# Performance work log

Measured on AMD Instinct MI355X. Metric: run time of the kernel, lower is better.

Reference implementation:

```python
import jax, jax.numpy as jnp
import numpy as np

B, S, D_IN, D_ST = 4, 4096, 1024, 1024


def setup_inputs() -> dict:
    key = jax.random.key(0)
    ks = jax.random.split(key, 7)
    s_in = 1.0 / np.sqrt(D_IN)
    s_st = 1.0 / np.sqrt(D_ST)
    return {
        "x": jax.random.normal(ks[0], (B, S, D_IN), dtype=jnp.float32),
        "gate_w": jax.random.uniform(ks[1], (D_IN, D_ST), jnp.float32, -s_in, s_in),
        "gate_b": jax.random.uniform(ks[2], (D_ST,), jnp.float32, -s_in, s_in),
        "inp_w": jax.random.uniform(ks[3], (D_IN, D_ST), jnp.float32, -s_in, s_in),
        "inp_b": jax.random.uniform(ks[4], (D_ST,), jnp.float32, -s_in, s_in),
        "out_w": jax.random.uniform(ks[5], (D_ST, D_IN), jnp.float32, -s_st, s_st),
        "out_b": jax.random.uniform(ks[6], (D_IN,), jnp.float32, -s_st, s_st),
    }


def reference(x, gate_w, gate_b, inp_w, inp_b, out_w, out_b):
    # x: [B, S, D_in]
    inp = jnp.einsum("bsd,de->bse", x, inp_w) + inp_b      # [B,S,Dst]
    gate = jax.nn.sigmoid(jnp.einsum("bsd,de->bse", x, gate_w) + gate_b)
    b_t = (1.0 - gate) * inp                               # [B,S,Dst]

    # affine recurrence h_t = gate_t * h_{t-1} + b_t via lax.scan over time
    def step(h, ab):
        a, b = ab
        h = a * h + b
        return h, h

    a_sb = jnp.swapaxes(gate, 0, 1)  # [S,B,Dst]
    b_sb = jnp.swapaxes(b_t, 0, 1)
    h0 = jnp.zeros((x.shape[0], inp.shape[-1]), dtype=x.dtype)
    _, hs = jax.lax.scan(step, h0, (a_sb, b_sb))           # [S,B,Dst]
    scan_out = jnp.swapaxes(hs, 0, 1)                      # [B,S,Dst]

    return x + jnp.einsum("bse,ed->bsd", scan_out, out_w) + out_b
```

## Files before the change

kernel.cpp:

```cpp
#include <hip/hip_runtime.h>

typedef unsigned short u16;
typedef unsigned int   u32;
typedef __bf16 bf16x8 __attribute__((ext_vector_type(8)));
typedef float  f32x4  __attribute__((ext_vector_type(4)));

#define DEVI __device__ __forceinline__

DEVI u16 f2bf(float f) {
    union { float f; u32 u; } c; c.f = f;
    u32 u = c.u;
    u32 r = (u + 0x7fffu + ((u >> 16) & 1u)) >> 16;
    return (u16)r;
}
DEVI float bf2f(u16 v) {
    union { u32 u; float f; } c; c.u = ((u32)v) << 16;
    return c.f;
}

DEVI void gload16(const void* g, void* l) {
    __builtin_amdgcn_global_load_lds(
        (const __attribute__((address_space(1))) void*)g,
        (__attribute__((address_space(3))) void*)l, 16, 0, 0);
}


#define VMW(N)  asm volatile("s_waitcnt vmcnt(" #N ")" ::: "memory")
#define BAR     __builtin_amdgcn_s_barrier()
#define SP1     __builtin_amdgcn_s_setprio(1)
#define SP0     __builtin_amdgcn_s_setprio(0)
#define CLOSE(N) __builtin_amdgcn_sched_barrier(0); VMW(N); BAR
#define CLOSEB   __builtin_amdgcn_sched_barrier(0); BAR

DEVI void stage_kh(const u16* g, u16* slot, int tid) {
    const int K = 1024;
    const int wvb = (tid >> 6) << 9;
    const int r = tid >> 2;
    const int p = tid & 3;
    const int c = p ^ (r & 3);
    const long off = (long)r * K + (c << 3);
    gload16(g + off, slot + wvb);
    gload16(g + off + (long)128 * K, slot + 4096 + wvb);
}

DEVI void ld4(bf16x8 (&d)[4], const u16* p) {
#pragma unroll
    for (int q = 0; q < 4; ++q) d[q] = *(const bf16x8*)(p + q * 512);
}
DEVI void mm16(f32x4 (&acc)[8][4], const bf16x8 a[4], const bf16x8 b[4], int mh) {
#pragma unroll
    for (int q = 0; q < 4; ++q)
#pragma unroll
        for (int n = 0; n < 4; ++n)
            acc[mh * 4 + q][n] =
                __builtin_amdgcn_mfma_f32_16x16x32_bf16(a[q], b[n], acc[mh * 4 + q][n], 0, 0, 0);
}

DEVI void pipeline(const u16* Ablk, const u16* Bblk, u16* lds,
                   f32x4 (&acc)[8][4], int tid) {
    const int lane = tid & 63;
    const int wm = (tid >> 6) >> 2, wn = (tid >> 6) & 3;
    const int pch = ((lane >> 4) ^ (lane & 3)) << 3;
    const int aoff = wm * 4096 + (lane & 15) * 32 + pch;
    const int boff = wn * 2048 + (lane & 15) * 32 + pch;

    stage_kh(Bblk,      lds + 16384, tid);
    stage_kh(Ablk,      lds + 0,     tid);
    stage_kh(Bblk + 32, lds + 24576, tid);
    stage_kh(Ablk + 32, lds + 8192,  tid);
    stage_kh(Bblk + 64, lds + 49152, tid);
    stage_kh(Ablk + 64, lds + 32768, tid);
    stage_kh(Bblk + 96, lds + 57344, tid);
    VMW(10); BAR;

    bf16x8 afA[4], afB[4], bfr[4];
    ld4(afA, lds + aoff);

#pragma unroll 1
    for (int j = 0; j < 7; ++j) {
        const u16* Aod = Ablk + (2 * j + 1) * 64;
        const u16* At2 = Ablk + (2 * j + 2) * 64;
        const u16* Bt2 = Bblk + (2 * j + 2) * 64;
        ld4(bfr, lds + 16384 + boff);
        ld4(afB, lds + 2048 + aoff);
        stage_kh(Aod + 32, lds + 40960, tid);
        SP1; mm16(acc, afA, bfr, 0); SP0; CLOSE(8);
        ld4(afA, lds + 8192 + aoff);
        stage_kh(Bt2, lds + 16384, tid);
        SP1; mm16(acc, afB, bfr, 1); SP0; CLOSE(8);
        ld4(bfr, lds + 24576 + boff);
        ld4(afB, lds + 10240 + aoff);
        stage_kh(At2, lds + 0, tid);
        SP1; mm16(acc, afA, bfr, 0); SP0; CLOSE(8);
        ld4(afA, lds + 32768 + aoff);
        stage_kh(Bt2 + 32, lds + 24576, tid);
        SP1; mm16(acc, afB, bfr, 1); SP0; CLOSE(8);
        ld4(bfr, lds + 49152 + boff);
        ld4(afB, lds + 34816 + aoff);
        stage_kh(At2 + 32, lds + 8192, tid);
        SP1; mm16(acc, afA, bfr, 0); SP0; CLOSE(8);
        ld4(afA, lds + 40960 + aoff);
        stage_kh(Bt2 + 64, lds + 49152, tid);
        SP1; mm16(acc, afB, bfr, 1); SP0; CLOSE(8);
        ld4(bfr, lds + 57344 + boff);
        ld4(afB, lds + 43008 + aoff);
        stage_kh(At2 + 64, lds + 32768, tid);
        SP1; mm16(acc, afA, bfr, 0); SP0; CLOSE(8);
        ld4(afA, lds + aoff);
        stage_kh(Bt2 + 96, lds + 57344, tid);
        SP1; mm16(acc, afB, bfr, 1); SP0; CLOSE(8);
    }
    {
        const u16* Aod = Ablk + 15 * 64;
        ld4(bfr, lds + 16384 + boff);
        ld4(afB, lds + 2048 + aoff);
        stage_kh(Aod + 32, lds + 40960, tid);
        SP1; mm16(acc, afA, bfr, 0); SP0; CLOSE(8);
        ld4(afA, lds + 8192 + aoff);
        SP1; mm16(acc, afB, bfr, 1); SP0; CLOSEB;
        ld4(bfr, lds + 24576 + boff);
        ld4(afB, lds + 10240 + aoff);
        SP1; mm16(acc, afA, bfr, 0); SP0; CLOSE(4);
        ld4(afA, lds + 32768 + aoff);
        SP1; mm16(acc, afB, bfr, 1); SP0; CLOSEB;
        ld4(bfr, lds + 49152 + boff);
        ld4(afB, lds + 34816 + aoff);
        SP1; mm16(acc, afA, bfr, 0); SP0; CLOSE(0);
        ld4(afA, lds + 40960 + aoff);
        SP1; mm16(acc, afB, bfr, 1); SP0; CLOSEB;
        ld4(bfr, lds + 57344 + boff);
        ld4(afB, lds + 43008 + aoff);
        SP1; mm16(acc, afA, bfr, 0); SP0; CLOSEB;
        SP1; mm16(acc, afB, bfr, 1); SP0;
    }
}


__global__ __launch_bounds__(512, 2) void k_gemm_cat8(
    const u16* __restrict__ A, const u16* __restrict__ Bcat,
    const float* __restrict__ gb, const float* __restrict__ ib,
    u32* __restrict__ ab) {
    __shared__ __align__(16) u16 lds[65536];
    const int tid = threadIdx.x, lane = tid & 63;
    const int wm = (tid >> 6) >> 2, wn = (tid >> 6) & 3;

    int fid = (int)blockIdx.y * 8 + (int)blockIdx.x;
    int swz = (fid & 7) * 64 + (fid >> 3);
    const long bn = swz & 7, bm = swz >> 3;

    f32x4 acc[8][4] = {};
    pipeline(A + bm * 256 * 1024, Bcat + bn * 256 * 1024, lds, acc, tid);

    const long rbase = bm * 256 + wm * 128;
    const int chbase = (int)bn * 128 + wn * 32;
#pragma unroll
    for (int t = 0; t < 2; ++t) {
        int ch = chbase + t * 16 + (lane & 15);
        float g0 = gb[ch], i0 = ib[ch];
#pragma unroll
        for (int m = 0; m < 8; ++m) {
            long row = rbase + m * 16 + ((lane >> 4) << 2);
#pragma unroll
            for (int i = 0; i < 4; ++i) {
                float pg = acc[m][2 * t][i] + g0;
                float pi = acc[m][2 * t + 1][i] + i0;
                float aa = 1.0f / (1.0f + __expf(-pg));
                float bb = (1.0f - aa) * pi;
                ab[(row + i) * 1024 + ch] = (u32)f2bf(aa) | ((u32)f2bf(bb) << 16);
            }
        }
    }
}


__global__ __launch_bounds__(512, 2) void k_gemm_out8(
    const u16* __restrict__ A, const u16* __restrict__ Bt,
    const float* __restrict__ xres, const float* __restrict__ ob,
    float* __restrict__ out) {
    __shared__ __align__(16) u16 lds[65536];
    const int tid = threadIdx.x, lane = tid & 63;
    const int wm = (tid >> 6) >> 2, wn = (tid >> 6) & 3;

    int fid = (int)blockIdx.y * 4 + (int)blockIdx.x;
    int swz = (fid & 7) * 32 + (fid >> 3);
    const long bn = swz & 3, bm = swz >> 2;

    f32x4 acc[8][4] = {};
    pipeline(A + bm * 256 * 1024, Bt + bn * 256 * 1024, lds, acc, tid);

    const long rbase = bm * 256 + wm * 128;
    const int cbase = (int)bn * 256 + wn * 64;
#pragma unroll
    for (int n = 0; n < 4; ++n) {
        int col = cbase + n * 16 + (lane & 15);
        float o0 = ob[col];
#pragma unroll
        for (int m = 0; m < 8; ++m) {
            long row = rbase + m * 16 + ((lane >> 4) << 2);
#pragma unroll
            for (int i = 0; i < 4; ++i) {
                long o = (row + i) * 1024 + col;
                out[o] = acc[m][n][i] + o0 + xres[o];
            }
        }
    }
}


__global__ __launch_bounds__(256) void k_cvt_x(const float4* __restrict__ x,
                                               uint2* __restrict__ o, int n4) {
    int i = blockIdx.x * 256 + threadIdx.x;
    if (i < n4) {
        float4 v = x[i];
        uint2 r;
        r.x = (u32)f2bf(v.x) | ((u32)f2bf(v.y) << 16);
        r.y = (u32)f2bf(v.z) | ((u32)f2bf(v.w) << 16);
        o[i] = r;
    }
}

__global__ __launch_bounds__(256) void k_transpose_bf(const float* __restrict__ w,
                                                      u16* __restrict__ wt, int R, int C) {
    __shared__ float t[32][33];
    int c0 = blockIdx.x * 32, r0 = blockIdx.y * 32;
    int x = threadIdx.x & 31, y = threadIdx.x >> 5;
    for (int i = y; i < 32; i += 8) t[i][x] = w[(size_t)(r0 + i) * C + c0 + x];
    __syncthreads();
    for (int i = y; i < 32; i += 8) wt[(size_t)(c0 + i) * R + r0 + x] = f2bf(t[x][i]);
}

__global__ __launch_bounds__(256) void k_transpose_cat(const float* __restrict__ gw,
                                                       const float* __restrict__ iw,
                                                       u16* __restrict__ wt, int K, int C) {
    __shared__ float t[32][33];
    int c0 = blockIdx.x * 32, r0 = blockIdx.y * 32;
    const float* w = blockIdx.z ? iw : gw;
    int x = threadIdx.x & 31, y = threadIdx.x >> 5;
    for (int i = y; i < 32; i += 8) t[i][x] = w[(size_t)(r0 + i) * C + c0 + x];
    __syncthreads();
    for (int i = y; i < 32; i += 8) {
        int ch = c0 + i;
        int r = ((ch >> 4) << 5) | ((int)blockIdx.z << 4) | (ch & 15);
        wt[(size_t)r * K + r0 + x] = f2bf(t[x][i]);
    }
}


__global__ __launch_bounds__(256) void k_scanA(const u32* __restrict__ ab,
                                               float2* __restrict__ cAB) {
    int e = blockIdx.x * 256 + threadIdx.x;
    int c = blockIdx.y, bt = blockIdx.z;
    long base = ((long)bt * 4096 + c * 64) * 1024 + e;
    float Aa = 1.f, H = 0.f;
#pragma unroll 4
    for (int i = 0; i < 64; ++i) {
        u32 v = ab[base + (long)i * 1024];
        float a = bf2f((u16)v), b = bf2f((u16)(v >> 16));
        H = a * H + b;
        Aa *= a;
    }
    cAB[((long)bt * 64 + c) * 1024 + e] = make_float2(Aa, H);
}

__global__ __launch_bounds__(256) void k_scanB(const float2* __restrict__ cAB,
                                               float* __restrict__ hin) {
    int e = blockIdx.x * 256 + threadIdx.x;
    int bt = blockIdx.y;
    float H = 0.f;
#pragma unroll
    for (int c = 0; c < 64; ++c) {
        long s = ((long)bt * 64 + c) * 1024 + e;
        hin[s] = H;
        float2 v = cAB[s];
        H = v.x * H + v.y;
    }
}

__global__ __launch_bounds__(256) void k_scanC(const u32* __restrict__ ab,
                                               const float* __restrict__ hin,
                                               u16* __restrict__ hout) {
    int e = blockIdx.x * 256 + threadIdx.x;
    int c = blockIdx.y, bt = blockIdx.z;
    long base = ((long)bt * 4096 + c * 64) * 1024 + e;
    float H = hin[((long)bt * 64 + c) * 1024 + e];
#pragma unroll 4
    for (int i = 0; i < 64; ++i) {
        u32 v = ab[base + (long)i * 1024];
        H = bf2f((u16)v) * H + bf2f((u16)(v >> 16));
        hout[base + (long)i * 1024] = f2bf(H);
    }
}


extern "C" void kernel_launch(void* const* d_in, const int* in_sizes, int n_in,
                              void* d_out, int out_size, void* d_ws, size_t ws_size,
                              hipStream_t stream) {
    const float* x      = (const float*)d_in[0];
    const float* gate_w = (const float*)d_in[1];
    const float* gate_b = (const float*)d_in[2];
    const float* inp_w  = (const float*)d_in[3];
    const float* inp_b  = (const float*)d_in[4];
    const float* out_w  = (const float*)d_in[5];
    const float* out_b  = (const float*)d_in[6];
    float* out = (float*)d_out;

    const int Bsz = 4, S = 4096, Din = 1024, Dst = 1024;
    const int M = Bsz * S;
    const long nx = (long)M * Din;

    char* w = (char*)d_ws;
    u16* xb      = (u16*)(w);
    u16* catW    = (u16*)(w + 33554432);
    u16* owT     = (u16*)(w + 37748736);
    u16* hbf     = (u16*)(w + 39845888);
    float2* cAB  = (float2*)(w + 73400320);
    float* hin   = (float*)(w + 75497472);

    u32* ab = (u32*)d_out;

    k_cvt_x<<<(int)(nx / 4 / 256), 256, 0, stream>>>((const float4*)x, (uint2*)xb, (int)(nx / 4));
    k_transpose_cat<<<dim3(Dst / 32, Din / 32, 2), 256, 0, stream>>>(gate_w, inp_w, catW, Din, Dst);
    k_transpose_bf<<<dim3(Din / 32, Dst / 32), 256, 0, stream>>>(out_w, owT, Dst, Din);

    k_gemm_cat8<<<dim3(8, M / 256), 512, 0, stream>>>(xb, catW, gate_b, inp_b, ab);

    k_scanA<<<dim3(4, 64, Bsz), 256, 0, stream>>>(ab, cAB);
    k_scanB<<<dim3(4, Bsz), 256, 0, stream>>>(cAB, hin);
    k_scanC<<<dim3(4, 64, Bsz), 256, 0, stream>>>(ab, hin, hbf);

    k_gemm_out8<<<dim3(4, M / 256), 512, 0, stream>>>(hbf, owT, x, out_b, out);
}
```

Baseline: 184.5 us.

## Replace deep LDS pipeline with double/triple-buffered loops and halve output GEMM tile

Replaces the hand-scheduled 8-slot LDS pipeline with simpler loops. The gate/input GEMM now double-buffers 32-wide K chunks with a full vmcnt(0) wait each step, while the output GEMM uses 128-row tiles with a three-stage ring and a smaller accumulator. The LDS footprint drops to 64KB or 72KB per block, and the output GEMM launches twice as many blocks, which targets occupancy and wave count on the GPU. The cost is shallower prefetch and a full memory wait per step, so global-load latency is hidden less.

```diff
diff --git a/kernel.cpp b/kernel.cpp
--- a/kernel.cpp
+++ b/kernel.cpp
@@ -26,21 +26,26 @@
 
 
 #define VMW(N)  asm volatile("s_waitcnt vmcnt(" #N ")" ::: "memory")
-#define BAR     __builtin_amdgcn_s_barrier()
+#define BARF    do { asm volatile("" ::: "memory"); __builtin_amdgcn_s_barrier(); \
+                     asm volatile("" ::: "memory"); } while (0)
 #define SP1     __builtin_amdgcn_s_setprio(1)
 #define SP0     __builtin_amdgcn_s_setprio(0)
-#define CLOSE(N) __builtin_amdgcn_sched_barrier(0); VMW(N); BAR
-#define CLOSEB   __builtin_amdgcn_sched_barrier(0); BAR
 
 DEVI void stage_kh(const u16* g, u16* slot, int tid) {
-    const int K = 1024;
     const int wvb = (tid >> 6) << 9;
     const int r = tid >> 2;
     const int p = tid & 3;
     const int c = p ^ (r & 3);
-    const long off = (long)r * K + (c << 3);
+    const long off = (long)r * 1024 + (c << 3);
     gload16(g + off, slot + wvb);
-    gload16(g + off + (long)128 * K, slot + 4096 + wvb);
+    gload16(g + off + (long)128 * 1024, slot + 4096 + wvb);
+}
+DEVI void stage_a128(const u16* g, u16* slot, int tid) {
+    const int wvb = (tid >> 6) << 9;
+    const int r = tid >> 2;
+    const int p = tid & 3;
+    const int c = p ^ (r & 3);
+    gload16(g + (long)r * 1024 + (c << 3), slot + wvb);
 }
 
 DEVI void ld4(bf16x8 (&d)[4], const u16* p) {
@@ -55,84 +60,95 @@
             acc[mh * 4 + q][n] =
                 __builtin_amdgcn_mfma_f32_16x16x32_bf16(a[q], b[n], acc[mh * 4 + q][n], 0, 0, 0);
 }
-
-DEVI void pipeline(const u16* Ablk, const u16* Bblk, u16* lds,
-                   f32x4 (&acc)[8][4], int tid) {
+DEVI void mm4(f32x4 (&acc)[4][4], const bf16x8 a[4], const bf16x8 b[4]) {
+#pragma unroll
+    for (int q = 0; q < 4; ++q)
+#pragma unroll
+        for (int n = 0; n < 4; ++n)
+            acc[q][n] =
+                __builtin_amdgcn_mfma_f32_16x16x32_bf16(a[q], b[n], acc[q][n], 0, 0, 0);
+}
+
+DEVI void pipe256(const u16* Ab, const u16* Bb, u16* lds,
+                  f32x4 (&acc)[8][4], int tid) {
     const int lane = tid & 63;
     const int wm = (tid >> 6) >> 2, wn = (tid >> 6) & 3;
     const int pch = ((lane >> 4) ^ (lane & 3)) << 3;
     const int aoff = wm * 4096 + (lane & 15) * 32 + pch;
-    const int boff = wn * 2048 + (lane & 15) * 32 + pch;
-
-    stage_kh(Bblk,      lds + 16384, tid);
-    stage_kh(Ablk,      lds + 0,     tid);
-    stage_kh(Bblk + 32, lds + 24576, tid);
-    stage_kh(Ablk + 32, lds + 8192,  tid);
-    stage_kh(Bblk + 64, lds + 49152, tid);
-    stage_kh(Ablk + 64, lds + 32768, tid);
-    stage_kh(Bblk + 96, lds + 57344, tid);
-    VMW(10); BAR;
-
-    bf16x8 afA[4], afB[4], bfr[4];
-    ld4(afA, lds + aoff);
-
+    const int boff = 8192 + wn * 2048 + (lane & 15) * 32 + pch;
+
+    stage_kh(Ab, lds, tid);
+    stage_kh(Bb, lds + 8192, tid);
+    VMW(0); BARF;
+
+    bf16x8 af0[4], af1[4], bfr[4];
 #pragma unroll 1
-    for (int j = 0; j < 7; ++j) {
-        const u16* Aod = Ablk + (2 * j + 1) * 64;
-        const u16* At2 = Ablk + (2 * j + 2) * 64;
-        const u16* Bt2 = Bblk + (2 * j + 2) * 64;
+    for (int j = 0; j < 15; ++j) {
+        const u16* gA1 = Ab + (2 * j + 1) * 32;
+        const u16* gB1 = Bb + (2 * j + 1) * 32;
+        const u16* gA2 = Ab + (2 * j + 2) * 32;
+        const u16* gB2 = Bb + (2 * j + 2) * 32;
+        stage_kh(gA1, lds + 16384, tid);
+        stage_kh(gB1, lds + 24576, tid);
+        ld4(bfr, lds + boff);
+        ld4(af0, lds + aoff);
+        ld4(af1, lds + 2048 + aoff);
+        SP1; mm16(acc, af0, bfr, 0); mm16(acc, af1, bfr, 1); SP0;
+        VMW(0); BARF;
+        stage_kh(gA2, lds, tid);
+        stage_kh(gB2, lds + 8192, tid);
         ld4(bfr, lds + 16384 + boff);
-        ld4(afB, lds + 2048 + aoff);
-        stage_kh(Aod + 32, lds + 40960, tid);
-        SP1; mm16(acc, afA, bfr, 0); SP0; CLOSE(8);
-        ld4(afA, lds + 8192 + aoff);
-        stage_kh(Bt2, lds + 16384, tid);
-        SP1; mm16(acc, afB, bfr, 1); SP0; CLOSE(8);
-        ld4(bfr, lds + 24576 + boff);
-        ld4(afB, lds + 10240 + aoff);
-        stage_kh(At2, lds + 0, tid);
-        SP1; mm16(acc, afA, bfr, 0); SP0; CLOSE(8);
-        ld4(afA, lds + 32768 + aoff);
-        stage_kh(Bt2 + 32, lds + 24576, tid);
-        SP1; mm16(acc, afB, bfr, 1); SP0; CLOSE(8);
-        ld4(bfr, lds + 49152 + boff);
-        ld4(afB, lds + 34816 + aoff);
-        stage_kh(At2 + 32, lds + 8192, tid);
-        SP1; mm16(acc, afA, bfr, 0); SP0; CLOSE(8);
-        ld4(afA, lds + 40960 + aoff);
-        stage_kh(Bt2 + 64, lds + 49152, tid);
-        SP1; mm16(acc, afB, bfr, 1); SP0; CLOSE(8);
-        ld4(bfr, lds + 57344 + boff);
-        ld4(afB, lds + 43008 + aoff);
-        stage_kh(At2 + 64, lds + 32768, tid);
-        SP1; mm16(acc, afA, bfr, 0); SP0; CLOSE(8);
-        ld4(afA, lds + aoff);
-        stage_kh(Bt2 + 96, lds + 57344, tid);
-        SP1; mm16(acc, afB, bfr, 1); SP0; CLOSE(8);
-    }
-    {
-        const u16* Aod = Ablk + 15 * 64;
-        ld4(bfr, lds + 16384 + boff);
-        ld4(afB, lds + 2048 + aoff);
-        stage_kh(Aod + 32, lds + 40960, tid);
-        SP1; mm16(acc, afA, bfr, 0); SP0; CLOSE(8);
-        ld4(afA, lds + 8192 + aoff);
-        SP1; mm16(acc, afB, bfr, 1); SP0; CLOSEB;
-        ld4(bfr, lds + 24576 + boff);
-        ld4(afB, lds + 10240 + aoff);
-        SP1; mm16(acc, afA, bfr, 0); SP0; CLOSE(4);
-        ld4(afA, lds + 32768 + aoff);
-        SP1; mm16(acc, afB, bfr, 1); SP0; CLOSEB;
-        ld4(bfr, lds + 49152 + boff);
-        ld4(afB, lds + 34816 + aoff);
-        SP1; mm16(acc, afA, bfr, 0); SP0; CLOSE(0);
-        ld4(afA, lds + 40960 + aoff);
-        SP1; mm16(acc, afB, bfr, 1); SP0; CLOSEB;
-        ld4(bfr, lds + 57344 + boff);
-        ld4(afB, lds + 43008 + aoff);
-        SP1; mm16(acc, afA, bfr, 0); SP0; CLOSEB;
-        SP1; mm16(acc, afB, bfr, 1); SP0;
-    }
+        ld4(af0, lds + 16384 + aoff);
+        ld4(af1, lds + 18432 + aoff);
+        SP1; mm16(acc, af0, bfr, 0); mm16(acc, af1, bfr, 1); SP0;
+        VMW(0); BARF;
+    }
+    stage_kh(Ab + 31 * 32, lds + 16384, tid);
+    stage_kh(Bb + 31 * 32, lds + 24576, tid);
+    ld4(bfr, lds + boff);
+    ld4(af0, lds + aoff);
+    ld4(af1, lds + 2048 + aoff);
+    SP1; mm16(acc, af0, bfr, 0); mm16(acc, af1, bfr, 1); SP0;
+    VMW(0); BARF;
+    ld4(bfr, lds + 16384 + boff);
+    ld4(af0, lds + 16384 + aoff);
+    ld4(af1, lds + 18432 + aoff);
+    SP1; mm16(acc, af0, bfr, 0); mm16(acc, af1, bfr, 1); SP0;
+}
+
+DEVI void pipe128(const u16* Ab, const u16* Bb, u16* lds,
+                  f32x4 (&acc)[4][4], int tid) {
+    const int lane = tid & 63;
+    const int wm = (tid >> 6) >> 2, wn = (tid >> 6) & 3;
+    const int pch = ((lane >> 4) ^ (lane & 3)) << 3;
+    const int aoff = wm * 2048 + (lane & 15) * 32 + pch;
+    const int boff = 4096 + wn * 2048 + (lane & 15) * 32 + pch;
+    u16* p0 = lds;
+    u16* p1 = lds + 12288;
+    u16* p2 = lds + 24576;
+
+    stage_a128(Ab, p0, tid);       stage_kh(Bb, p0 + 4096, tid);
+    stage_a128(Ab + 32, p1, tid);  stage_kh(Bb + 32, p1 + 4096, tid);
+    VMW(3); BARF;
+
+    bf16x8 af[4], bfr[4];
+#pragma unroll 1
+    for (int t = 0; t < 30; ++t) {
+        stage_a128(Ab + (t + 2) * 32, p2, tid);
+        stage_kh(Bb + (t + 2) * 32, p2 + 4096, tid);
+        ld4(bfr, p0 + boff);
+        ld4(af, p0 + aoff);
+        SP1; mm4(acc, af, bfr); SP0;
+        VMW(3); BARF;
+        u16* tmp = p0; p0 = p1; p1 = p2; p2 = tmp;
+    }
+    ld4(bfr, p0 + boff);
+    ld4(af, p0 + aoff);
+    SP1; mm4(acc, af, bfr); SP0;
+    VMW(0); BARF;
+    ld4(bfr, p1 + boff);
+    ld4(af, p1 + aoff);
+    SP1; mm4(acc, af, bfr); SP0;
 }
 
 
@@ -140,7 +156,7 @@
     const u16* __restrict__ A, const u16* __restrict__ Bcat,
     const float* __restrict__ gb, const float* __restrict__ ib,
     u32* __restrict__ ab) {
-    __shared__ __align__(16) u16 lds[65536];
+    __shared__ __align__(16) u16 lds[32768];
     const int tid = threadIdx.x, lane = tid & 63;
     const int wm = (tid >> 6) >> 2, wn = (tid >> 6) & 3;
 
@@ -149,7 +165,7 @@
     const long bn = swz & 7, bm = swz >> 3;
 
     f32x4 acc[8][4] = {};
-    pipeline(A + bm * 256 * 1024, Bcat + bn * 256 * 1024, lds, acc, tid);
+    pipe256(A + bm * 256 * 1024, Bcat + bn * 256 * 1024, lds, acc, tid);
 
     const long rbase = bm * 256 + wm * 128;
     const int chbase = (int)bn * 128 + wn * 32;
@@ -177,25 +193,25 @@
     const u16* __restrict__ A, const u16* __restrict__ Bt,
     const float* __restrict__ xres, const float* __restrict__ ob,
     float* __restrict__ out) {
-    __shared__ __align__(16) u16 lds[65536];
+    __shared__ __align__(16) u16 lds[36864];
     const int tid = threadIdx.x, lane = tid & 63;
     const int wm = (tid >> 6) >> 2, wn = (tid >> 6) & 3;
 
     int fid = (int)blockIdx.y * 4 + (int)blockIdx.x;
-    int swz = (fid & 7) * 32 + (fid >> 3);
+    int swz = (fid & 7) * 64 + (fid >> 3);
     const long bn = swz & 3, bm = swz >> 2;
 
-    f32x4 acc[8][4] = {};
-    pipeline(A + bm * 256 * 1024, Bt + bn * 256 * 1024, lds, acc, tid);
-
-    const long rbase = bm * 256 + wm * 128;
+    f32x4 acc[4][4] = {};
+    pipe128(A + bm * 128 * 1024, Bt + bn * 256 * 1024, lds, acc, tid);
+
+    const long rbase = bm * 128 + wm * 64;
     const int cbase = (int)bn * 256 + wn * 64;
 #pragma unroll
     for (int n = 0; n < 4; ++n) {
         int col = cbase + n * 16 + (lane & 15);
         float o0 = ob[col];
 #pragma unroll
-        for (int m = 0; m < 8; ++m) {
+        for (int m = 0; m < 4; ++m) {
             long row = rbase + m * 16 + ((lane >> 4) << 2);
 #pragma unroll
             for (int i = 0; i < 4; ++i) {
@@ -328,5 +344,5 @@
     k_scanB<<<dim3(4, Bsz), 256, 0, stream>>>(cAB, hin);
     k_scanC<<<dim3(4, 64, Bsz), 256, 0, stream>>>(ab, hin, hbf);
 
-    k_gemm_out8<<<dim3(4, M / 256), 512, 0, stream>>>(hbf, owT, x, out_b, out);
-}
+    k_gemm_out8<<<dim3(4, M / 128), 512, 0, stream>>>(hbf, owT, x, out_b, out);
+}
```

After: 183.1 us. About the same (-0.8%).

## Restructure GEMM main loop into 8-phase double-buffered pipeline with register-held B fragments

Applied to the files above, without the earlier changes.

Replaces the old K-step pipeline with a macro-generated 8-phase schedule. Each 64-wide K tile's B fragments are loaded once into registers and reused across four A sub-phases. Staging now moves whole K=64 tiles into two LDS halves, with explicit lgkmcnt/vmcnt waits and barriers around each MFMA burst. Launch bounds drop from 2 to 1 blocks per CU, which frees registers for the larger fragment set but removes the second resident block that could hide latency.

```diff
diff --git a/kernel.cpp b/kernel.cpp
--- a/kernel.cpp
+++ b/kernel.cpp
@@ -29,114 +29,116 @@
 #define BAR     __builtin_amdgcn_s_barrier()
 #define SP1     __builtin_amdgcn_s_setprio(1)
 #define SP0     __builtin_amdgcn_s_setprio(0)
-#define CLOSE(N) __builtin_amdgcn_sched_barrier(0); VMW(N); BAR
-#define CLOSEB   __builtin_amdgcn_sched_barrier(0); BAR
+#define SCB     __builtin_amdgcn_sched_barrier(0)
+#define LGKM0   asm volatile("s_waitcnt lgkmcnt(0)" ::: "memory")
+#define LGKM8   asm volatile("s_waitcnt lgkmcnt(8)" ::: "memory")
 
 DEVI void stage_kh(const u16* g, u16* slot, int tid) {
-    const int K = 1024;
     const int wvb = (tid >> 6) << 9;
     const int r = tid >> 2;
     const int p = tid & 3;
     const int c = p ^ (r & 3);
-    const long off = (long)r * K + (c << 3);
+    const long off = (long)r * 1024 + (c << 3);
     gload16(g + off, slot + wvb);
-    gload16(g + off + (long)128 * K, slot + 4096 + wvb);
-}
-
-DEVI void ld4(bf16x8 (&d)[4], const u16* p) {
-#pragma unroll
-    for (int q = 0; q < 4; ++q) d[q] = *(const bf16x8*)(p + q * 512);
-}
-DEVI void mm16(f32x4 (&acc)[8][4], const bf16x8 a[4], const bf16x8 b[4], int mh) {
-#pragma unroll
-    for (int q = 0; q < 4; ++q)
-#pragma unroll
-        for (int n = 0; n < 4; ++n)
-            acc[mh * 4 + q][n] =
-                __builtin_amdgcn_mfma_f32_16x16x32_bf16(a[q], b[n], acc[mh * 4 + q][n], 0, 0, 0);
-}
-
-DEVI void pipeline(const u16* Ablk, const u16* Bblk, u16* lds,
-                   f32x4 (&acc)[8][4], int tid) {
+    gload16(g + off + (long)128 * 1024, slot + 4096 + wvb);
+}
+
+DEVI f32x4 mfma(const bf16x8& a, const bf16x8& b, const f32x4& c) {
+    return __builtin_amdgcn_mfma_f32_16x16x32_bf16(a, b, c, 0, 0, 0);
+}
+
+#define PHASE(I, Q, STAGE_CODE, GATE_CODE)                                   \
+    {                                                                        \
+        if (I == 0) {                                                        \
+            _Pragma("unroll")                                                \
+            for (int nf = 0; nf < 4; ++nf) {                                 \
+                bh[nf][0] = *(const bf16x8*)(lds + (Q) + 16384 + nf * 512 + bbase); \
+                bh[nf][1] = *(const bf16x8*)(lds + (Q) + 24576 + nf * 512 + bbase); \
+            }                                                                \
+        }                                                                    \
+        a00 = *(const bf16x8*)(lds + (Q) + (I) * 1024 + abase);              \
+        a01 = *(const bf16x8*)(lds + (Q) + 8192 + (I) * 1024 + abase);       \
+        a10 = *(const bf16x8*)(lds + (Q) + (I) * 1024 + 512 + abase);        \
+        a11 = *(const bf16x8*)(lds + (Q) + 8192 + (I) * 1024 + 512 + abase); \
+        if (I == 0) { LGKM8; }                                               \
+        STAGE_CODE;                                                          \
+        SCB; BAR;                                                            \
+        LGKM0; SCB;                                                          \
+        SP1;                                                                 \
+        _Pragma("unroll")                                                    \
+        for (int nf = 0; nf < 4; ++nf) {                                     \
+            acc[(I) * 2][nf]     = mfma(a00, bh[nf][0], acc[(I) * 2][nf]);   \
+            acc[(I) * 2][nf]     = mfma(a01, bh[nf][1], acc[(I) * 2][nf]);   \
+            acc[(I) * 2 + 1][nf] = mfma(a10, bh[nf][0], acc[(I) * 2 + 1][nf]); \
+            acc[(I) * 2 + 1][nf] = mfma(a11, bh[nf][1], acc[(I) * 2 + 1][nf]); \
+        }                                                                    \
+        SP0;                                                                 \
+        GATE_CODE;                                                           \
+        BAR;                                                                 \
+    }
+
+#define NOSTAGE do {} while (0)
+#define NOGATE  do {} while (0)
+
+DEVI void pipe256(const u16* Ab, const u16* Bb, u16* lds,
+                  f32x4 (&acc)[8][4], int tid) {
     const int lane = tid & 63;
     const int wm = (tid >> 6) >> 2, wn = (tid >> 6) & 3;
     const int pch = ((lane >> 4) ^ (lane & 3)) << 3;
-    const int aoff = wm * 4096 + (lane & 15) * 32 + pch;
-    const int boff = wn * 2048 + (lane & 15) * 32 + pch;
-
-    stage_kh(Bblk,      lds + 16384, tid);
-    stage_kh(Ablk,      lds + 0,     tid);
-    stage_kh(Bblk + 32, lds + 24576, tid);
-    stage_kh(Ablk + 32, lds + 8192,  tid);
-    stage_kh(Bblk + 64, lds + 49152, tid);
-    stage_kh(Ablk + 64, lds + 32768, tid);
-    stage_kh(Bblk + 96, lds + 57344, tid);
-    VMW(10); BAR;
-
-    bf16x8 afA[4], afB[4], bfr[4];
-    ld4(afA, lds + aoff);
+    const int abase = (wm * 128 + (lane & 15)) * 32 + pch;
+    const int bbase = (wn * 64 + (lane & 15)) * 32 + pch;
+
+    stage_kh(Bb,      lds + 16384, tid);
+    stage_kh(Bb + 32, lds + 24576, tid);
+    stage_kh(Ab,      lds + 0,     tid);
+    stage_kh(Ab + 32, lds + 8192,  tid);
+    stage_kh(Bb + 64, lds + 49152, tid);
+    stage_kh(Bb + 96, lds + 57344, tid);
+    VMW(4); BAR;
+
+    bf16x8 bh[4][2];
+    bf16x8 a00, a01, a10, a11;
 
 #pragma unroll 1
     for (int j = 0; j < 7; ++j) {
-        const u16* Aod = Ablk + (2 * j + 1) * 64;
-        const u16* At2 = Ablk + (2 * j + 2) * 64;
-        const u16* Bt2 = Bblk + (2 * j + 2) * 64;
-        ld4(bfr, lds + 16384 + boff);
-        ld4(afB, lds + 2048 + aoff);
-        stage_kh(Aod + 32, lds + 40960, tid);
-        SP1; mm16(acc, afA, bfr, 0); SP0; CLOSE(8);
-        ld4(afA, lds + 8192 + aoff);
-        stage_kh(Bt2, lds + 16384, tid);
-        SP1; mm16(acc, afB, bfr, 1); SP0; CLOSE(8);
-        ld4(bfr, lds + 24576 + boff);
-        ld4(afB, lds + 10240 + aoff);
-        stage_kh(At2, lds + 0, tid);
-        SP1; mm16(acc, afA, bfr, 0); SP0; CLOSE(8);
-        ld4(afA, lds + 32768 + aoff);
-        stage_kh(Bt2 + 32, lds + 24576, tid);
-        SP1; mm16(acc, afB, bfr, 1); SP0; CLOSE(8);
-        ld4(bfr, lds + 49152 + boff);
-        ld4(afB, lds + 34816 + aoff);
-        stage_kh(At2 + 32, lds + 8192, tid);
-        SP1; mm16(acc, afA, bfr, 0); SP0; CLOSE(8);
-        ld4(afA, lds + 40960 + aoff);
-        stage_kh(Bt2 + 64, lds + 49152, tid);
-        SP1; mm16(acc, afB, bfr, 1); SP0; CLOSE(8);
-        ld4(bfr, lds + 57344 + boff);
-        ld4(afB, lds + 43008 + aoff);
-        stage_kh(At2 + 64, lds + 32768, tid);
-        SP1; mm16(acc, afA, bfr, 0); SP0; CLOSE(8);
-        ld4(afA, lds + aoff);
-        stage_kh(Bt2 + 96, lds + 57344, tid);
-        SP1; mm16(acc, afB, bfr, 1); SP0; CLOSE(8);
+        const u16* A1g = Ab + (2 * j + 1) * 64;
+        const u16* A2g = Ab + (2 * j + 2) * 64;
+        const u16* B2g = Bb + (2 * j + 2) * 64;
+        const u16* B3g = Bb + (2 * j + 3) * 64;
+        PHASE(0, 0,
+              { stage_kh(A1g, lds + 32768, tid); stage_kh(A1g + 32, lds + 40960, tid); },
+              NOGATE);
+        PHASE(1, 0,
+              { stage_kh(B2g, lds + 16384, tid); stage_kh(B2g + 32, lds + 24576, tid); },
+              NOGATE);
+        PHASE(2, 0, NOSTAGE, NOGATE);
+        PHASE(3, 0, NOSTAGE, VMW(4));
+        PHASE(0, 32768,
+              { stage_kh(A2g, lds + 0, tid); stage_kh(A2g + 32, lds + 8192, tid); },
+              NOGATE);
+        PHASE(1, 32768,
+              { stage_kh(B3g, lds + 49152, tid); stage_kh(B3g + 32, lds + 57344, tid); },
+              NOGATE);
+        PHASE(2, 32768, NOSTAGE, NOGATE);
+        PHASE(3, 32768, NOSTAGE, VMW(4));
     }
     {
-        const u16* Aod = Ablk + 15 * 64;
-        ld4(bfr, lds + 16384 + boff);
-        ld4(afB, lds + 2048 + aoff);
-        stage_kh(Aod + 32, lds + 40960, tid);
-        SP1; mm16(acc, afA, bfr, 0); SP0; CLOSE(8);
-        ld4(afA, lds + 8192 + aoff);
-        SP1; mm16(acc, afB, bfr, 1); SP0; CLOSEB;
-        ld4(bfr, lds + 24576 + boff);
-        ld4(afB, lds + 10240 + aoff);
-        SP1; mm16(acc, afA, bfr, 0); SP0; CLOSE(4);
-        ld4(afA, lds + 32768 + aoff);
-        SP1; mm16(acc, afB, bfr, 1); SP0; CLOSEB;
-        ld4(bfr, lds + 49152 + boff);
-        ld4(afB, lds + 34816 + aoff);
-        SP1; mm16(acc, afA, bfr, 0); SP0; CLOSE(0);
-        ld4(afA, lds + 40960 + aoff);
-        SP1; mm16(acc, afB, bfr, 1); SP0; CLOSEB;
-        ld4(bfr, lds + 57344 + boff);
-        ld4(afB, lds + 43008 + aoff);
-        SP1; mm16(acc, afA, bfr, 0); SP0; CLOSEB;
-        SP1; mm16(acc, afB, bfr, 1); SP0;
-    }
-}
-
-
-__global__ __launch_bounds__(512, 2) void k_gemm_cat8(
+        const u16* A15 = Ab + 15 * 64;
+        PHASE(0, 0,
+              { stage_kh(A15, lds + 32768, tid); stage_kh(A15 + 32, lds + 40960, tid); },
+              NOGATE);
+        PHASE(1, 0, NOSTAGE, NOGATE);
+        PHASE(2, 0, NOSTAGE, NOGATE);
+        PHASE(3, 0, NOSTAGE, VMW(0));
+        PHASE(0, 32768, NOSTAGE, NOGATE);
+        PHASE(1, 32768, NOSTAGE, NOGATE);
+        PHASE(2, 32768, NOSTAGE, NOGATE);
+        PHASE(3, 32768, NOSTAGE, NOGATE);
+    }
+}
+
+
+__global__ __launch_bounds__(512, 1) void k_gemm_cat8(
     const u16* __restrict__ A, const u16* __restrict__ Bcat,
     const float* __restrict__ gb, const float* __restrict__ ib,
     u32* __restrict__ ab) {
@@ -149,7 +151,7 @@
     const long bn = swz & 7, bm = swz >> 3;
 
     f32x4 acc[8][4] = {};
-    pipeline(A + bm * 256 * 1024, Bcat + bn * 256 * 1024, lds, acc, tid);
+    pipe256(A + bm * 256 * 1024, Bcat + bn * 256 * 1024, lds, acc, tid);
 
     const long rbase = bm * 256 + wm * 128;
     const int chbase = (int)bn * 128 + wn * 32;
@@ -173,7 +175,7 @@
 }
 
 
-__global__ __launch_bounds__(512, 2) void k_gemm_out8(
+__global__ __launch_bounds__(512, 1) void k_gemm_out8(
     const u16* __restrict__ A, const u16* __restrict__ Bt,
     const float* __restrict__ xres, const float* __restrict__ ob,
     float* __restrict__ out) {
@@ -186,7 +188,7 @@
     const long bn = swz & 3, bm = swz >> 2;
 
     f32x4 acc[8][4] = {};
-    pipeline(A + bm * 256 * 1024, Bt + bn * 256 * 1024, lds, acc, tid);
+    pipe256(A + bm * 256 * 1024, Bt + bn * 256 * 1024, lds, acc, tid);
 
     const long rbase = bm * 256 + wm * 128;
     const int cbase = (int)bn * 256 + wn * 64;
```

Measured after the change: 187.5 us. Within noise of the previous version (+1.6%).
